# Performance work log

Hardware: AMD Instinct MI355X
Metric: run time of the kernel (lower is better)

Reference implementation:

```python
import jax, jax.numpy as jnp
import numpy as np

B, S, HID = 2, 2048, 2048
H = 16
Q_LORA = 1536
KV_LORA = 512
NOPE = 128
ROPE = 64
VDIM = 128
EPS = 1e-6
THETA = 10000.0
SCALE = 1.0 / np.sqrt(NOPE + ROPE)


def rmsnorm(x, w):
    var = jnp.mean(jnp.square(x), axis=-1, keepdims=True)
    return x * jax.lax.rsqrt(var + EPS) * w


def rotate_half(x):
    x1, x2 = jnp.split(x, 2, axis=-1)
    return jnp.concatenate([-x2, x1], axis=-1)


def setup_inputs() -> dict:
    key = jax.random.key(0)
    ks = jax.random.split(key, 10)
    w = 0.02
    hidden_states = jax.random.normal(ks[0], (B, S, HID), jnp.float32)
    # causal additive mask (bsz, 1, q_len, kv_len)
    causal = jnp.tril(jnp.ones((S, S), jnp.bool_))
    attention_mask = jnp.where(causal, 0.0, jnp.finfo(jnp.float32).min)[None, None].repeat(B, 0)
    position_ids = jnp.broadcast_to(jnp.arange(S, dtype=jnp.int64), (B, S))
    return {
        'hidden_states': hidden_states,
        'attention_mask': attention_mask,
        'q_a_w': jax.random.normal(ks[1], (Q_LORA, HID), jnp.float32) * w,
        'q_a_ln_w': jnp.ones((Q_LORA,), jnp.float32),
        'q_b_rope_w': jax.random.normal(ks[2], (H * ROPE, Q_LORA), jnp.float32) * w,
        'qk_nope_w': jax.random.normal(ks[3], (H * KV_LORA, Q_LORA), jnp.float32) * w,
        'kv_a_w': jax.random.normal(ks[4], (KV_LORA + ROPE, HID), jnp.float32) * w,
        'kv_a_ln_w': jnp.ones((KV_LORA,), jnp.float32),
        'v_b_w': jax.random.normal(ks[5], (H * VDIM, KV_LORA), jnp.float32) * w,
        'o_w': jax.random.normal(ks[6], (HID, H * VDIM), jnp.float32) * w,
        'position_ids': position_ids,
    }


def reference(hidden_states, attention_mask, q_a_w, q_a_ln_w, q_b_rope_w, qk_nope_w,
              kv_a_w, kv_a_ln_w, v_b_w, o_w, position_ids):
    b, s, _ = hidden_states.shape
    # low-rank Q path
    q_a = rmsnorm(hidden_states @ q_a_w.T, q_a_ln_w)                 # (b,s,Q_LORA)
    q_rope = (q_a @ q_b_rope_w.T).reshape(b, s, H, ROPE).transpose(0, 2, 1, 3)  # (b,h,s,rd)
    # compressed KV + shared rope key
    ckv_full = hidden_states @ kv_a_w.T                              # (b,s,KV_LORA+ROPE)
    ckv = rmsnorm(ckv_full[..., :KV_LORA], kv_a_ln_w)                # (b,s,KV_LORA)
    k_rope = ckv_full[..., KV_LORA:]                                 # (b,s,rd)
    # rotary embedding
    inv_freq = 1.0 / (THETA ** (jnp.arange(0, ROPE, 2, dtype=jnp.float32) / ROPE))
    t = jnp.arange(s, dtype=jnp.float32)
    freqs = jnp.outer(t, inv_freq)                                   # (s, rd/2)
    emb = jnp.concatenate([freqs, freqs], axis=-1)                   # (s, rd)
    cos = jnp.cos(emb)[position_ids][:, None]                        # (b,1,s,rd)
    sin = jnp.sin(emb)[position_ids][:, None]
    q_rope = q_rope * cos + rotate_half(q_rope) * sin                # (b,h,s,rd)
    k_rope = k_rope[:, None] * cos + rotate_half(k_rope[:, None]) * sin  # (b,1,s,rd)
    # absorbed nope score: q_a -> (b,h,s,KV_LORA) then vs compressed kv
    nope_q = (q_a @ qk_nope_w.T).reshape(b, s, H, KV_LORA).transpose(0, 2, 1, 3)
    nope_score = jnp.einsum('bhqc,bkc->bhqk', nope_q, ckv)
    rope_score = jnp.einsum('bhqr,bkr->bhqk', q_rope, k_rope[:, 0])
    attn = (nope_score + rope_score) * SCALE + attention_mask
    attn = jax.nn.softmax(attn.astype(jnp.float32), axis=-1).astype(hidden_states.dtype)
    # AV in compressed space, then absorbed v projection
    ctx = jnp.einsum('bhqk,bkc->bhqc', attn, ckv)                    # (b,h,q,KV_LORA)
    v_w = v_b_w.reshape(H, VDIM, KV_LORA)
    out = jnp.einsum('bhqc,hvc->bhqv', ctx, v_w)                     # (b,h,q,VDIM)
    out = out.transpose(0, 2, 1, 3).reshape(b, s, H * VDIM)
    return out @ o_w.T
```

## Files before the change

kernel.cpp:

```cpp
#include <hip/hip_runtime.h>
#include <hip/hip_bf16.h>

typedef __bf16 bf16;
typedef __bf16 bf16x8 __attribute__((ext_vector_type(8)));
typedef float f32x4 __attribute__((ext_vector_type(4)));
typedef float f32x16 __attribute__((ext_vector_type(16)));

#define AS3(p) ((__attribute__((address_space(3))) void*)(p))
#define AS1(p) ((const __attribute__((address_space(1))) void*)(p))
#define GLDS16(g,l) __builtin_amdgcn_global_load_lds(AS1(g), AS3(l), 16, 0, 0)
#define MFMA_BF16(a,b,c) __builtin_amdgcn_mfma_f32_16x16x32_bf16((a),(b),(c),0,0,0)
#define MFMA32(a,b,c) __builtin_amdgcn_mfma_f32_32x32x16_bf16((a),(b),(c),0,0,0)

constexpr int S_ = 2048;
constexpr int H_ = 16;
constexpr int KVL_ = 512;
constexpr int ROPE_ = 64;
constexpr int VD_ = 128;
constexpr int DQK_ = 576;
constexpr int QKV_N = 2176;
constexpr float SCALE_ = 0.07216878364870323f;

__device__ __forceinline__ bf16 to_bf16(float f) {
    unsigned u = __builtin_bit_cast(unsigned, f);
    unsigned r = u + 0x7FFFu + ((u >> 16) & 1u);
    unsigned short h = (unsigned short)(r >> 16);
    return __builtin_bit_cast(bf16, h);
}

__device__ __forceinline__ unsigned cvt_pk_bf16(float lo, float hi) {
    unsigned r;
    asm("v_cvt_pk_bf16_f32 %0, %1, %2" : "=v"(r) : "v"(lo), "v"(hi));
    return r;
}

__global__ void cast_all_kernel(const float* __restrict__ s0, const float* __restrict__ s1,
                                const float* __restrict__ s2, const float* __restrict__ s3,
                                const float* __restrict__ s4, const float* __restrict__ s5,
                                const float* __restrict__ s6,
                                bf16* __restrict__ d0, bf16* __restrict__ d1, bf16* __restrict__ d2,
                                bf16* __restrict__ d3, bf16* __restrict__ d4, bf16* __restrict__ d5,
                                bf16* __restrict__ d6) {
    constexpr long ns[7]  = {8388608L, 3145728L, 1179648L, 1572864L, 12582912L, 1048576L, 4194304L};
    constexpr long pds[7] = {8388608L, 3145728L, 1310720L, 1572864L, 12582912L, 1048576L, 4194304L};
    const int seg = blockIdx.y;
    const float* in = (seg == 0) ? s0 : (seg == 1) ? s1 : (seg == 2) ? s2 : (seg == 3) ? s3
                    : (seg == 4) ? s4 : (seg == 5) ? s5 : s6;
    bf16* out = (seg == 0) ? d0 : (seg == 1) ? d1 : (seg == 2) ? d2 : (seg == 3) ? d3
              : (seg == 4) ? d4 : (seg == 5) ? d5 : d6;
    const long n = ns[seg], pad = pds[seg];
    long i = ((long)blockIdx.x * 256 + threadIdx.x) * 4;
    const long stride = (long)gridDim.x * 256 * 4;
    for (; i < pad; i += stride) {
        if (i < n) {
            float4 v = *(const float4*)(in + i);
            out[i + 0] = to_bf16(v.x); out[i + 1] = to_bf16(v.y);
            out[i + 2] = to_bf16(v.z); out[i + 3] = to_bf16(v.w);
        } else {
            out[i + 0] = to_bf16(0.f); out[i + 1] = to_bf16(0.f);
            out[i + 2] = to_bf16(0.f); out[i + 3] = to_bf16(0.f);
        }
    }
}

__global__ void rope_table_kernel(float* __restrict__ cosT, float* __restrict__ sinT) {
    int idx = blockIdx.x * 256 + threadIdx.x;
    if (idx >= S_ * 32) return;
    int s = idx >> 5, j = idx & 31;
    float invf = expf(-(float)(2 * j) * (1.0f / 64.0f) * 9.210340371976184f);
    float a = (float)s * invf;
    cosT[idx] = cosf(a);
    sinT[idx] = sinf(a);
}

__global__ void fused_post_kernel(const float* __restrict__ scr, const float* __restrict__ qw,
                                  const float* __restrict__ kw, const float* __restrict__ cosT,
                                  const float* __restrict__ sinT, bf16* __restrict__ qab,
                                  bf16* __restrict__ ckvb, bf16* __restrict__ krb) {
    const int row = blockIdx.x;
    const int tid = threadIdx.x;
    const float* x = scr + (long)row * QKV_N;
    float ssq = 0.f, ssk = 0.f;
    for (int i = tid; i < 1536; i += 256) { float v = x[i]; ssq += v * v; }
    for (int i = tid; i < 512; i += 256) { float v = x[1536 + i]; ssk += v * v; }
#pragma unroll
    for (int d = 1; d < 64; d <<= 1) { ssq += __shfl_xor(ssq, d); ssk += __shfl_xor(ssk, d); }
    __shared__ float rq[4], rk[4];
    if ((tid & 63) == 0) { rq[tid >> 6] = ssq; rk[tid >> 6] = ssk; }
    __syncthreads();
    float rsq = rsqrtf((rq[0] + rq[1] + rq[2] + rq[3]) / 1536.f + 1e-6f);
    float rsk = rsqrtf((rk[0] + rk[1] + rk[2] + rk[3]) / 512.f + 1e-6f);
    for (int i = tid; i < 1536; i += 256)
        qab[(long)row * 1536 + i] = to_bf16(x[i] * rsq * qw[i]);
    for (int i = tid; i < 512; i += 256)
        ckvb[(long)row * 512 + i] = to_bf16(x[1536 + i] * rsk * kw[i]);
    if (tid < 64) {
        int s = row & (S_ - 1);
        const float* kr = x + 2048;
        float other = (tid < 32) ? -kr[tid + 32] : kr[tid - 32];
        float c = cosT[s * 32 + (tid & 31)], sn = sinT[s * 32 + (tid & 31)];
        krb[(long)row * 64 + tid] = to_bf16(kr[tid] * c + other * sn);
    }
}

template <int MODE>
__global__ __launch_bounds__(256, 2)
void gemm_bt_kernel(const bf16* __restrict__ A, const bf16* __restrict__ Bm,
                    void* __restrict__ Cout, int M, int N, int K,
                    const float* __restrict__ cosT = nullptr,
                    const float* __restrict__ sinT = nullptr) {
    constexpr int BK = 32;
    __shared__ bf16 As[2][128 * BK];
    __shared__ bf16 Bs[2][128 * BK];
    const int tid = threadIdx.x;
    const int w = tid >> 6;
    const int lane = tid & 63;
    const int nwg = gridDim.x * gridDim.y;
    const int lin = blockIdx.y * gridDim.x + blockIdx.x;
    const int swz = (lin & 7) * (nwg >> 3) + (lin >> 3);
    const long m0 = (long)(swz % gridDim.x) * 128;
    const long n0 = (long)(swz / gridDim.x) * 128;
    const int wm = (w >> 1) * 64, wn = (w & 1) * 64;
    const int lr = lane & 15;
    const int lk = (lane >> 4) * 8;

    const int c0 = w * 2, c1 = w * 2 + 1;
    const int srow0 = c0 * 16 + (lane >> 2);
    const int srow1 = c1 * 16 + (lane >> 2);
    const int skc = (lane & 3) * 8;
    const bf16* ga0 = A + (m0 + srow0) * (long)K + skc;
    const bf16* ga1 = A + (m0 + srow1) * (long)K + skc;
    const bf16* gb0 = Bm + (n0 + srow0) * (long)K + skc;
    const bf16* gb1 = Bm + (n0 + srow1) * (long)K + skc;

#define GSTAGE(p) do { \
    GLDS16(ga0, &As[p][c0 * 512]); \
    GLDS16(gb0, &Bs[p][c0 * 512]); \
    GLDS16(ga1, &As[p][c1 * 512]); \
    GLDS16(gb1, &Bs[p][c1 * 512]); \
    ga0 += BK; ga1 += BK; gb0 += BK; gb1 += BK; \
} while (0)

    f32x4 acc[4][4] = {};
    const int nT = K / BK;

    GSTAGE(0);
    __syncthreads();

    for (int t = 0; t < nT; ++t) {
        const int p = t & 1;
        if (t + 1 < nT) GSTAGE(p ^ 1);
        bf16x8 av[4], bv[4];
#pragma unroll
        for (int i = 0; i < 4; i++) av[i] = *(const bf16x8*)&As[p][(wm + i * 16 + lr) * BK + lk];
#pragma unroll
        for (int j = 0; j < 4; j++) bv[j] = *(const bf16x8*)&Bs[p][(wn + j * 16 + lr) * BK + lk];
#pragma unroll
        for (int i = 0; i < 4; i++)
#pragma unroll
            for (int j = 0; j < 4; j++)
                acc[i][j] = MFMA_BF16(av[i], bv[j], acc[i][j]);
        __syncthreads();
    }
#undef GSTAGE

    const int r4 = (lane >> 4) * 4;
    if (MODE == 3) {
#pragma unroll
        for (int i = 0; i < 4; i++)
#pragma unroll
            for (int r = 0; r < 4; r++) {
                long gm = m0 + wm + i * 16 + r4 + r;
                int s = (int)(gm & (S_ - 1));
#pragma unroll
                for (int j = 0; j < 2; j++) {
                    float c = cosT[s * 32 + j * 16 + lr];
                    float sn = sinT[s * 32 + j * 16 + lr];
                    float lo = acc[i][j][r], hiv = acc[i][j + 2][r];
                    long gn = n0 + wn + j * 16 + lr;
                    ((bf16*)Cout)[gm * 1024 + gn] = to_bf16((lo * c - hiv * sn) * SCALE_);
                    ((bf16*)Cout)[gm * 1024 + gn + 32] = to_bf16((hiv * c + lo * sn) * SCALE_);
                }
            }
        return;
    }
#pragma unroll
    for (int i = 0; i < 4; i++)
#pragma unroll
        for (int j = 0; j < 4; j++) {
            long gmb = m0 + wm + i * 16 + r4;
            long gn = n0 + wn + j * 16 + lr;
#pragma unroll
            for (int r = 0; r < 4; r++) {
                long gm = gmb + r;
                float v = acc[i][j][r];
                if (MODE == 0) {
                    if (gn < N) ((float*)Cout)[gm * N + gn] = v;
                } else if (MODE == 1) {
                    if (gn < N) ((bf16*)Cout)[gm * N + gn] = to_bf16(v * SCALE_);
                } else {
                    long idx = (gm >> 11) * (2048L * 2048) + gn * 2048 + (gm & 2047);
                    ((bf16*)Cout)[idx] = to_bf16(v);
                }
            }
        }
}

__global__ __launch_bounds__(256, 2)
void flash_kernel(const bf16* __restrict__ nopeq, const bf16* __restrict__ ropeq,
                  const bf16* __restrict__ ckv, const bf16* __restrict__ krope,
                  const bf16* __restrict__ vt, bf16* __restrict__ outa) {
    __shared__ bf16 Ks2[32 * 512];
    __shared__ bf16 Krs[32 * 64];
    __shared__ char VtsB[10240];
    __shared__ char PldsB[4][32 * 80];
    const int tid = threadIdx.x;
    const int w = tid >> 6, lane = tid & 63;
    const int l31 = lane & 31;
    const int hi = lane >> 5;
    const int kel = hi * 8;
    const int klo = hi * 16;
    const int h = blockIdx.y, b = blockIdx.z;
    const int xq = (b == 0) ? (int)blockIdx.x : (15 - (int)blockIdx.x);
    const int q0 = xq * 128;
    const long bS = (long)b * S_;
    const int qg = q0 + (l31 << 2) + w;
    const int kvoff = hi * 4;

    bf16x8 qf[36];
    {
        const bf16* np = nopeq + (bS + qg) * (long)(H_ * KVL_) + h * KVL_;
        const bf16* rp = ropeq + (bS + qg) * (long)(H_ * ROPE_) + h * ROPE_;
#pragma unroll
        for (int t = 0; t < 32; ++t) qf[t] = *(const bf16x8*)(np + t * 16 + kel);
#pragma unroll
        for (int t = 0; t < 4; ++t) qf[32 + t] = *(const bf16x8*)(rp + t * 16 + kel);
    }

    unsigned soff[12];
#pragma unroll
    for (int k = 0; k < 8; ++k) {
        int c = w + 4 * k;
        soff[k] = (unsigned)((bS + c) * 1024 + ((lane * 16) ^ ((c & 7) << 4)));
    }
    {
        int rr = w * 8 + (lane >> 3);
        soff[8] = (unsigned)((bS + rr) * 128 + (((lane & 7) * 16) ^ ((rr & 7) << 4)));
    }
#pragma unroll
    for (int k = 9; k < 12; ++k) {
        int cc = (k == 11) ? (8 + w) : (w + 4 * (k - 9));
        int byt = cc * 1024 + lane * 16;
        int v = byt / 80, col = byt - v * 80;
        soff[k] = (col < 64) ? (unsigned)((((long)(b * H_ + h) * VD_ + v) * S_ + (col >> 1)) * 2) : 0u;
    }

    f32x16 accv[4] = {};
    float m_run = -3e38f, l_run = 0.f;
    const int nkv = q0 / 32 + 4;
    const int kswz = (l31 & 7) << 4;

    for (int it = 0; it < nkv; ++it) {
        const int kv0 = it * 32;
        __syncthreads();
#pragma unroll
        for (int k = 0; k < 8; ++k) {
            GLDS16((const char*)ckv + soff[k], (char*)Ks2 + (w + 4 * k) * 1024);
            soff[k] += 32768;
        }
        GLDS16((const char*)krope + soff[8], (char*)Krs + w * 1024);
        soff[8] += 4096;
        GLDS16((const char*)vt + soff[9], VtsB + w * 1024); soff[9] += 64;
        GLDS16((const char*)vt + soff[10], VtsB + (w + 4) * 1024); soff[10] += 64;
        if (w < 2) { GLDS16((const char*)vt + soff[11], VtsB + (8 + w) * 1024); soff[11] += 64; }
        __syncthreads();

        f32x16 sc = {};
        __builtin_amdgcn_s_setprio(1);
#pragma unroll
        for (int t = 0; t < 32; ++t) {
            bf16x8 kf = *(const bf16x8*)((const char*)Ks2 + l31 * 1024 + ((t * 32 + klo) ^ kswz));
            sc = MFMA32(kf, qf[t], sc);
        }
#pragma unroll
        for (int t = 0; t < 4; ++t) {
            bf16x8 kf = *(const bf16x8*)((const char*)Krs + l31 * 128 + ((t * 32 + klo) ^ kswz));
            sc = MFMA32(kf, qf[32 + t], sc);
        }
        __builtin_amdgcn_s_setprio(0);

        float s[16];
        if (kv0 + 31 > q0 + w) {
#pragma unroll
            for (int r = 0; r < 16; ++r) {
                int kvg = kv0 + kvoff + ((r & 3) + 8 * (r >> 2));
                s[r] = (kvg > qg) ? -3e38f : sc[r];
            }
        } else {
#pragma unroll
            for (int r = 0; r < 16; ++r) s[r] = sc[r];
        }

        float m8[8];
#pragma unroll
        for (int r = 0; r < 8; ++r) m8[r] = fmaxf(s[r], s[r + 8]);
        float m4a = fmaxf(m8[0], m8[1]), m4b = fmaxf(m8[2], m8[3]);
        float m4c = fmaxf(m8[4], m8[5]), m4d = fmaxf(m8[6], m8[7]);
        float mx = fmaxf(fmaxf(m4a, m4b), fmaxf(m4c, m4d));
        mx = fmaxf(mx, __shfl_xor(mx, 32));

        float mnew = fmaxf(m_run, mx);
        float corr = __expf(m_run - mnew);
#pragma unroll
        for (int r = 0; r < 16; ++r) s[r] = __expf(s[r] - mnew);
        float r8[8];
#pragma unroll
        for (int r = 0; r < 8; ++r) r8[r] = s[r] + s[r + 8];
        float r4a = r8[0] + r8[1], r4b = r8[2] + r8[3], r4c = r8[4] + r8[5], r4d = r8[6] + r8[7];
        float rs = (r4a + r4b) + (r4c + r4d);
        rs += __shfl_xor(rs, 32);

        if (__any(mnew > m_run)) {
#pragma unroll
            for (int vg = 0; vg < 4; ++vg)
#pragma unroll
                for (int r = 0; r < 16; ++r) accv[vg][r] *= corr;
        }
        l_run = l_run * corr + rs;
        m_run = mnew;

        {
            char* prow = PldsB[w] + l31 * 80;
#pragma unroll
            for (int g = 0; g < 4; ++g) {
                uint2 pk;
                pk.x = cvt_pk_bf16(s[4 * g + 0], s[4 * g + 1]);
                pk.y = cvt_pk_bf16(s[4 * g + 2], s[4 * g + 3]);
                *(uint2*)(prow + g * 16 + 8 * hi) = pk;
            }
        }
        bf16x8 pfrag[2];
#pragma unroll
        for (int c = 0; c < 2; ++c)
            pfrag[c] = *(const bf16x8*)(PldsB[w] + l31 * 80 + c * 32 + klo);

        __builtin_amdgcn_s_setprio(1);
#pragma unroll
        for (int c = 0; c < 2; ++c) {
#pragma unroll
            for (int vg = 0; vg < 4; ++vg) {
                bf16x8 vf = *(const bf16x8*)(VtsB + (vg * 32 + l31) * 80 + c * 32 + klo);
                accv[vg] = MFMA32(vf, pfrag[c], accv[vg]);
            }
        }
        __builtin_amdgcn_s_setprio(0);
    }

    float invl = 1.f / l_run;
    bf16* orow = outa + (bS + qg) * (long)(H_ * VD_) + h * VD_;
#pragma unroll
    for (int vg = 0; vg < 4; ++vg)
#pragma unroll
        for (int rq = 0; rq < 4; ++rq) {
            int vb = vg * 32 + rq * 8 + kvoff;
            ushort4 u;
            u.x = __builtin_bit_cast(unsigned short, to_bf16(accv[vg][rq * 4 + 0] * invl));
            u.y = __builtin_bit_cast(unsigned short, to_bf16(accv[vg][rq * 4 + 1] * invl));
            u.z = __builtin_bit_cast(unsigned short, to_bf16(accv[vg][rq * 4 + 2] * invl));
            u.w = __builtin_bit_cast(unsigned short, to_bf16(accv[vg][rq * 4 + 3] * invl));
            *(ushort4*)(orow + vb) = u;
        }
}

extern "C" void kernel_launch(void* const* d_in, const int* in_sizes, int n_in,
                              void* d_out, int out_size, void* d_ws, size_t ws_size,
                              hipStream_t stream) {
    const float* hidden     = (const float*)d_in[0];
    const float* q_a_w      = (const float*)d_in[2];
    const float* q_a_ln_w   = (const float*)d_in[3];
    const float* q_b_rope_w = (const float*)d_in[4];
    const float* qk_nope_w  = (const float*)d_in[5];
    const float* kv_a_w     = (const float*)d_in[6];
    const float* kv_a_ln_w  = (const float*)d_in[7];
    const float* v_b_w      = (const float*)d_in[8];
    const float* o_w        = (const float*)d_in[9];

    char* ws = (char*)d_ws;
    size_t off = 0;
    auto alloc = [&](size_t bytes) -> void* {
        void* p = ws + off;
        off += (bytes + 255) & ~(size_t)255;
        return p;
    };
    bf16* hb     = (bf16*)alloc(4096L * 2048 * 2);
    bf16* wqakv  = (bf16*)alloc((long)QKV_N * 2048 * 2);
    bf16* wqr    = (bf16*)alloc(1024L * 1536 * 2);
    bf16* wnp    = (bf16*)alloc(8192L * 1536 * 2);
    bf16* wvb    = (bf16*)alloc(2048L * 512 * 2);
    bf16* wo     = (bf16*)alloc(2048L * 2048 * 2);
    float* f32scr = (float*)alloc(4096L * QKV_N * 4);
    bf16* qab    = (bf16*)alloc(4096L * 1536 * 2);
    bf16* qrb    = (bf16*)alloc(4096L * 1024 * 2);
    bf16* npq    = (bf16*)alloc(4096L * 8192 * 2);
    bf16* ckvb   = (bf16*)alloc(4096L * 512 * 2);
    bf16* krb    = (bf16*)alloc(4096L * 64 * 2);
    bf16* vtb    = (bf16*)alloc(2L * 2048 * 2048 * 2);
    bf16* aout   = (bf16*)alloc(4096L * 2048 * 2);
    float* cosT  = (float*)alloc(2048L * 32 * 4);
    float* sinT  = (float*)alloc(2048L * 32 * 4);
    (void)ws_size; (void)in_sizes; (void)n_in; (void)out_size;

    cast_all_kernel<<<dim3(512, 7), 256, 0, stream>>>(
        hidden, q_a_w, kv_a_w, q_b_rope_w, qk_nope_w, v_b_w, o_w,
        hb, wqakv, wqakv + 1536L * 2048, wqr, wnp, wvb, wo);
    rope_table_kernel<<<256, 256, 0, stream>>>(cosT, sinT);

    gemm_bt_kernel<0><<<dim3(32, 17), 256, 0, stream>>>(hb, wqakv, f32scr, 4096, QKV_N, 2048);
    fused_post_kernel<<<4096, 256, 0, stream>>>(f32scr, q_a_ln_w, kv_a_ln_w, cosT, sinT, qab, ckvb, krb);
    gemm_bt_kernel<3><<<dim3(32, 8), 256, 0, stream>>>(qab, wqr, qrb, 4096, 1024, 1536, cosT, sinT);
    gemm_bt_kernel<1><<<dim3(32, 64), 256, 0, stream>>>(qab, wnp, npq, 4096, 8192, 1536);
    gemm_bt_kernel<2><<<dim3(32, 16), 256, 0, stream>>>(ckvb, wvb, vtb, 4096, 2048, 512);
    flash_kernel<<<dim3(16, 16, 2), 256, 0, stream>>>(npq, qrb, ckvb, krb, vtb, aout);
    gemm_bt_kernel<0><<<dim3(32, 16), 256, 0, stream>>>(aout, wo, (float*)d_out, 4096, 2048, 2048);
}
```

Measured before the change: 587.1 us.

## Triple-buffer GEMM LDS stages with explicit vmcnt waits and vectorize transposed stores

The bf16 GEMM kernel moves from a double-buffered LDS pipeline with __syncthreads to a three-stage ring, issuing loads two tiles ahead and waiting on vmcnt counts before a raw s_barrier. The goal is to hide global-to-LDS latency better and avoid draining every outstanding load at each iteration. The MODE 2 transposed epilogue now packs four consecutive bf16 values into one 8-byte store instead of four scalar stores. The cost is more LDS per block, which may limit occupancy, plus hand-written waitcnt logic that is only correct if each stage issues exactly four loads.

```diff
diff --git a/kernel.cpp b/kernel.cpp
--- a/kernel.cpp
+++ b/kernel.cpp
@@ -11,6 +11,7 @@
 #define GLDS16(g,l) __builtin_amdgcn_global_load_lds(AS1(g), AS3(l), 16, 0, 0)
 #define MFMA_BF16(a,b,c) __builtin_amdgcn_mfma_f32_16x16x32_bf16((a),(b),(c),0,0,0)
 #define MFMA32(a,b,c) __builtin_amdgcn_mfma_f32_32x32x16_bf16((a),(b),(c),0,0,0)
+#define SCHED_FENCE() do { __builtin_amdgcn_sched_barrier(0); asm volatile("" ::: "memory"); } while (0)
 
 constexpr int S_ = 2048;
 constexpr int H_ = 16;
@@ -26,6 +27,12 @@
     unsigned r = u + 0x7FFFu + ((u >> 16) & 1u);
     unsigned short h = (unsigned short)(r >> 16);
     return __builtin_bit_cast(bf16, h);
+}
+
+__device__ __forceinline__ unsigned short bf16bits(float f) {
+    unsigned u = __builtin_bit_cast(unsigned, f);
+    unsigned r = u + 0x7FFFu + ((u >> 16) & 1u);
+    return (unsigned short)(r >> 16);
 }
 
 __device__ __forceinline__ unsigned cvt_pk_bf16(float lo, float hi) {
@@ -110,8 +117,8 @@
                     const float* __restrict__ cosT = nullptr,
                     const float* __restrict__ sinT = nullptr) {
     constexpr int BK = 32;
-    __shared__ bf16 As[2][128 * BK];
-    __shared__ bf16 Bs[2][128 * BK];
+    __shared__ bf16 As[3][128 * BK];
+    __shared__ bf16 Bs[3][128 * BK];
     const int tid = threadIdx.x;
     const int w = tid >> 6;
     const int lane = tid & 63;
@@ -145,11 +152,19 @@
     const int nT = K / BK;
 
     GSTAGE(0);
-    __syncthreads();
+    if (nT > 1) {
+        GSTAGE(1);
+        asm volatile("s_waitcnt vmcnt(4)" ::: "memory");
+    } else {
+        asm volatile("s_waitcnt vmcnt(0)" ::: "memory");
+    }
+    SCHED_FENCE();
+    __builtin_amdgcn_s_barrier();
+    SCHED_FENCE();
 
     for (int t = 0; t < nT; ++t) {
-        const int p = t & 1;
-        if (t + 1 < nT) GSTAGE(p ^ 1);
+        const int p = t % 3;
+        if (t + 2 < nT) GSTAGE((t + 2) % 3);
         bf16x8 av[4], bv[4];
 #pragma unroll
         for (int i = 0; i < 4; i++) av[i] = *(const bf16x8*)&As[p][(wm + i * 16 + lr) * BK + lk];
@@ -160,7 +175,14 @@
 #pragma unroll
             for (int j = 0; j < 4; j++)
                 acc[i][j] = MFMA_BF16(av[i], bv[j], acc[i][j]);
-        __syncthreads();
+        if (t + 1 < nT) {
+            SCHED_FENCE();
+            if (t + 2 < nT) asm volatile("s_waitcnt vmcnt(4)" ::: "memory");
+            else            asm volatile("s_waitcnt vmcnt(0)" ::: "memory");
+            SCHED_FENCE();
+            __builtin_amdgcn_s_barrier();
+            SCHED_FENCE();
+        }
     }
 #undef GSTAGE
 
@@ -190,17 +212,24 @@
         for (int j = 0; j < 4; j++) {
             long gmb = m0 + wm + i * 16 + r4;
             long gn = n0 + wn + j * 16 + lr;
-#pragma unroll
-            for (int r = 0; r < 4; r++) {
-                long gm = gmb + r;
-                float v = acc[i][j][r];
-                if (MODE == 0) {
-                    if (gn < N) ((float*)Cout)[gm * N + gn] = v;
-                } else if (MODE == 1) {
-                    if (gn < N) ((bf16*)Cout)[gm * N + gn] = to_bf16(v * SCALE_);
-                } else {
-                    long idx = (gm >> 11) * (2048L * 2048) + gn * 2048 + (gm & 2047);
-                    ((bf16*)Cout)[idx] = to_bf16(v);
+            if (MODE == 2) {
+                long idx = (gmb >> 11) * (2048L * 2048) + gn * 2048 + (gmb & 2047);
+                ushort4 u;
+                u.x = bf16bits(acc[i][j][0]);
+                u.y = bf16bits(acc[i][j][1]);
+                u.z = bf16bits(acc[i][j][2]);
+                u.w = bf16bits(acc[i][j][3]);
+                *(ushort4*)((bf16*)Cout + idx) = u;
+            } else {
+#pragma unroll
+                for (int r = 0; r < 4; r++) {
+                    long gm = gmb + r;
+                    float v = acc[i][j][r];
+                    if (MODE == 0) {
+                        if (gn < N) ((float*)Cout)[gm * N + gn] = v;
+                    } else {
+                        if (gn < N) ((bf16*)Cout)[gm * N + gn] = to_bf16(v * SCALE_);
+                    }
                 }
             }
         }
```

New measurement: 589.9 us. Within noise of the previous version (+0.5%).
